# Kernel optimization log

Hardware: AMD Instinct MI355X
Metric: run time of the kernel (lower is better)

Reference implementation:

```python
import jax, jax.numpy as jnp
import numpy as np
from jax import lax

B, CIN, H, W = 4096, 3, 64, 64
NVAR = 50

def _lin(x, w, b):
    return jax.nn.relu(x @ w + b)

def setup_inputs() -> dict:
    key = jax.random.key(0)
    ks = jax.random.split(key, 16)
    def rn(k, shape, scale=0.05):
        return jax.random.normal(k, shape, dtype=jnp.float32) * scale
    return {
        "x": jax.random.normal(ks[0], (B, CIN, H, W), dtype=jnp.float32),
        "C": jax.random.uniform(ks[1], (B, NVAR, NVAR), dtype=jnp.float32),
        "conv1_w": rn(ks[2], (32, CIN, 3, 3)), "conv1_b": jnp.zeros((32,), jnp.float32),
        "conv2_w": rn(ks[3], (64, 32, 3, 3)), "conv2_b": jnp.zeros((64,), jnp.float32),
        "enc_w": rn(ks[4], (64, 128)), "enc_b": jnp.zeros((128,), jnp.float32),
        "f1_w": rn(ks[5], (128, NVAR)), "f1_b": jnp.zeros((NVAR,), jnp.float32),
        "f2_w": rn(ks[6], (NVAR, 128)), "f2_b": jnp.zeros((128,), jnp.float32),
        "f3_w": rn(ks[7], (256, 64)), "f3_b": jnp.zeros((64,), jnp.float32),
        "f4_w": rn(ks[8], (64, 64)), "f4_b": jnp.zeros((64,), jnp.float32),
        "f5_w": rn(ks[9], (64, 64)), "f5_b": jnp.zeros((64,), jnp.float32),
        "out_w": rn(ks[10], (64, NVAR)), "out_b": jnp.zeros((NVAR,), jnp.float32),
    }

def reference(x, C, conv1_w, conv1_b, conv2_w, conv2_b, enc_w, enc_b,
              f1_w, f1_b, f2_w, f2_b, f3_w, f3_b, f4_w, f4_b, f5_w, f5_b,
              out_w, out_b):
    dn = ("NCHW", "OIHW", "NCHW")
    # Observation_Encoder_F: conv(s2)->relu->conv(s2)->relu->global mean pool->linear->relu
    h = lax.conv_general_dilated(x, conv1_w, (2, 2), ((1, 1), (1, 1)), dimension_numbers=dn)
    h = jax.nn.relu(h + conv1_b[None, :, None, None])          # [B,32,32,32]
    h = lax.conv_general_dilated(h, conv2_w, (2, 2), ((1, 1), (1, 1)), dimension_numbers=dn)
    h = jax.nn.relu(h + conv2_b[None, :, None, None])          # [B,64,16,16]
    x1 = _lin(h.mean(axis=(2, 3)), enc_w, enc_b)               # [B,128]
    x2 = _lin(x1, f1_w, f1_b)                                  # [B,V]
    # per-sample causal matrix multiply: e[b] = C[b] @ x2[b]
    e = jnp.einsum("bij,bj->bi", C, x2)                        # [B,V]
    x3 = _lin(e, f2_w, f2_b)                                   # [B,128]
    x4 = jnp.concatenate((x1, x3), axis=1)                     # [B,256]
    x5 = _lin(x4, f3_w, f3_b)
    x6 = _lin(x5, f4_w, f4_b)
    x7 = _lin(x6, f5_w, f5_b)
    return jax.nn.softmax(_lin(x7, out_w, out_b), axis=1)      # [B,V]
```

## Files before the change

### kernel.cpp

```cpp
#include <hip/hip_runtime.h>
#include <hip/hip_bf16.h>


typedef __attribute__((ext_vector_type(8)))  short short8;
typedef __attribute__((ext_vector_type(16))) float floatx16;

#define AS1 __attribute__((address_space(1)))
#define AS3 __attribute__((address_space(3)))

#define BAR_LGKM() asm volatile("s_waitcnt lgkmcnt(0)\ns_barrier" ::: "memory")
#define BAR_FULL() asm volatile("s_waitcnt vmcnt(0) lgkmcnt(0)\ns_barrier" ::: "memory")

__device__ __forceinline__ short f2bf(float f) {
    unsigned u = __float_as_uint(f);
    u += 0x7fffu + ((u >> 16) & 1u);
    return (short)(u >> 16);
}

__device__ __forceinline__ float rl(float v, int i) {
    return __int_as_float(__builtin_amdgcn_readlane(__float_as_int(v), i));
}

__device__ __forceinline__ unsigned pkbf2(float a, float b) {
    float2 fp; fp.x = a; fp.y = b;
    __hip_bfloat162 bb = __float22bfloat162_rn(fp);
    return *(unsigned*)&bb;
}

__global__ void k_prep(const float* __restrict__ cw2, const float* __restrict__ cw1,
                       short* __restrict__ packw) {
    const int idx = blockIdx.x * 256 + threadIdx.x;
    if (idx < 9 * 64 * 32) {
        const int ic  = idx & 31;
        const int oc  = (idx >> 5) & 63;
        const int pos = idx >> 11;
        packw[idx] = f2bf(cw2[oc * 288 + ic * 9 + pos]);
    } else if (idx < 9 * 64 * 32 + 32 * 32) {
        const int j  = idx - 9 * 64 * 32;
        const int k  = j & 31;
        const int oc = j >> 5;
        packw[idx] = (k < 27) ? f2bf(cw1[oc * 27 + k]) : (short)0;
    }
}

#define XS_OFF  0
#define A1_OFF  49152
#define A1STR   80
#define H1_OFF  90112
#define ROWB    2064
#define SMEM_SZ (49152 + 40960 + 66048)
#define SPB     16

__global__ __launch_bounds__(256, 1) void k_conv(
    const float* __restrict__ x,    const float* __restrict__ c1b,
    const short* __restrict__ packw, const float* __restrict__ c2b,
    float* __restrict__ pooled)
{
    __shared__ __align__(16) char smem[SMEM_SZ];
    float* xs      = (float*)(smem + XS_OFF);
    char*  a1      = smem + A1_OFF;
    char*  h1b     = smem + H1_OFF;
    float* poolbuf = (float*)(smem + A1_OFF);

    const int tid  = threadIdx.x;
    const int lane = tid & 63;
    const int w    = tid >> 6;

    const int col = lane & 31;
    const int ss  = lane >> 5;

    const int nt  = w & 1;
    const int mh  = w >> 1;
    const int ox2 = lane & 15;
    const int oyb = (lane >> 4) & 1;
    const int ocn = nt * 32 + col;
    const float bias2 = c2b[ocn];
    const float bias1 = c1b[col];

    short8 z8;
    #pragma unroll
    for (int i = 0; i < 8; ++i) z8[i] = 0;

    short8 bfr[9][2];
    #pragma unroll
    for (int pos = 0; pos < 9; ++pos)
        #pragma unroll
        for (int h = 0; h < 2; ++h)
            bfr[pos][h] = *(const short8*)(packw + (pos * 64 + ocn) * 32 + h * 16 + ss * 8);

    const short* w1p = packw + 18432;
    short8 w1f[2];
    #pragma unroll
    for (int k = 0; k < 2; ++k)
        w1f[k] = *(const short8*)(w1p + col * 32 + k * 16 + ss * 8);

    auto prefetch_x = [&](int bb) {
        const char* g = (const char*)(x + (size_t)bb * 12288);
        #pragma unroll
        for (int i = 0; i < 12; ++i) {
            const int off = (w * 12 + i) << 10;
            __builtin_amdgcn_global_load_lds(
                (const AS1 unsigned int*)(g + off + lane * 16),
                (AS3 unsigned int*)(smem + XS_OFF + off), 16, 0, 0);
        }
    };

    auto im2col = [&](int half) {
        #pragma unroll
        for (int px = 0; px < 2; ++px) {
            const int p  = tid + px * 256;
            const int oy = half * 16 + (p >> 5);
            const int ox = p & 31;
            float f[32];
            #pragma unroll
            for (int ic = 0; ic < 3; ++ic) {
                #pragma unroll
                for (int ky = 0; ky < 3; ++ky) {
                    const int  iy   = 2 * oy + ky - 1;
                    const bool oky  = iy >= 0;
                    const int  base = ic * 4096 + (oky ? iy : 0) * 64 + 2 * ox;
                    const float2 p12 = *(const float2*)(xs + base);
                    const float  v0  = xs[(base > 0) ? base - 1 : 0];
                    const int k = ic * 9 + ky * 3;
                    f[k + 0] = (oky && ox > 0) ? v0 : 0.f;
                    f[k + 1] = oky ? p12.x : 0.f;
                    f[k + 2] = oky ? p12.y : 0.f;
                }
            }
            f[27] = 0.f; f[28] = 0.f; f[29] = 0.f; f[30] = 0.f; f[31] = 0.f;
            unsigned pk[16];
            #pragma unroll
            for (int t = 0; t < 16; ++t) pk[t] = pkbf2(f[2 * t], f[2 * t + 1]);
            uint4* dst = (uint4*)(a1 + p * A1STR);
            dst[0] = make_uint4(pk[0],  pk[1],  pk[2],  pk[3]);
            dst[1] = make_uint4(pk[4],  pk[5],  pk[6],  pk[7]);
            dst[2] = make_uint4(pk[8],  pk[9],  pk[10], pk[11]);
            dst[3] = make_uint4(pk[12], pk[13], pk[14], pk[15]);
        }
    };

    auto conv1_mfma = [&](int half) {
        #pragma unroll
        for (int i = 0; i < 4; ++i) {
            const int t = w * 4 + i;
            const char* abase = a1 + (t * 32 + col) * A1STR + ss * 16;
            const short8 af0 = *(const short8*)(abase);
            const short8 af1 = *(const short8*)(abase + 32);
            floatx16 acc;
            #pragma unroll
            for (int r = 0; r < 16; ++r) acc[r] = 0.f;
            acc = __builtin_amdgcn_mfma_f32_32x32x16_bf16(af0, w1f[0], acc, 0, 0, 0);
            acc = __builtin_amdgcn_mfma_f32_32x32x16_bf16(af1, w1f[1], acc, 0, 0, 0);
            const int oyg = half * 16 + t;
            char* hb = h1b + oyg * ROWB + col * 2;
            #pragma unroll
            for (int r = 0; r < 16; r += 2) {
                const int row = (r & 3) + 8 * (r >> 2) + 4 * ss;
                const unsigned u = pkbf2(fmaxf(acc[r]     + bias1, 0.f),
                                         fmaxf(acc[r + 1] + bias1, 0.f));
                *(unsigned short*)(hb + (row >> 1) * 64)        = (unsigned short)u;
                *(unsigned short*)(hb + (row >> 1) * 64 + 1024) = (unsigned short)(u >> 16);
            }
        }
    };

    prefetch_x(blockIdx.x);

    #pragma unroll 1
    for (int s = 0; s < SPB; ++s) {
        const int b = blockIdx.x + (s << 8);

        BAR_FULL();
        im2col(0);
        BAR_LGKM();
        conv1_mfma(0);
        BAR_LGKM();
        im2col(1);
        BAR_LGKM();
        if (s + 1 < SPB) prefetch_x(blockIdx.x + ((s + 1) << 8));
        conv1_mfma(1);
        BAR_LGKM();

        float pool = 0.f;
        #pragma unroll
        for (int tp = 0; tp < 2; ++tp) {
            const int t0 = mh * 4 + tp * 2;
            floatx16 acc0, acc1;
            #pragma unroll
            for (int r = 0; r < 16; ++r) { acc0[r] = 0.f; acc1[r] = 0.f; }
            #pragma unroll
            for (int ky = 0; ky < 3; ++ky) {
                #pragma unroll
                for (int kx = 0; kx < 3; ++kx) {
                    const int  iy0 = t0 * 4 + oyb * 2 + ky - 1;
                    const int  ph  = (kx + 1) & 1;
                    const int  xh  = ox2 - (kx == 0 ? 1 : 0);
                    const bool okx = (xh >= 0);
                    const bool ok0 = okx && (iy0 >= 0);
                    const int  sb  = (ph * 16 + xh) * 64 + ss * 16;
                    const int  ba0 = iy0 * ROWB + sb;
                    const int  ba1 = ba0 + 4 * ROWB;
                    #pragma unroll
                    for (int h = 0; h < 2; ++h) {
                        short8 a0v = ok0 ? *(const short8*)(h1b + ba0 + h * 32) : z8;
                        short8 a1v = okx ? *(const short8*)(h1b + ba1 + h * 32) : z8;
                        const short8 bf = bfr[ky * 3 + kx][h];
                        acc0 = __builtin_amdgcn_mfma_f32_32x32x16_bf16(a0v, bf, acc0, 0, 0, 0);
                        acc1 = __builtin_amdgcn_mfma_f32_32x32x16_bf16(a1v, bf, acc1, 0, 0, 0);
                    }
                }
            }
            #pragma unroll
            for (int r = 0; r < 16; ++r) {
                pool += fmaxf(acc0[r] + bias2, 0.f);
                pool += fmaxf(acc1[r] + bias2, 0.f);
            }
        }
        pool += __shfl_xor(pool, 32, 64);
        if (lane < 32) poolbuf[w * 32 + lane] = pool;
        BAR_LGKM();
        if (tid < 64) {
            const int g = tid >> 5, c = tid & 31;
            pooled[(size_t)b * 64 + tid] =
                (poolbuf[g * 32 + c] + poolbuf[(g + 2) * 32 + c]) * (1.f / 256.f);
        }
    }
}

__global__ __launch_bounds__(256, 4) void k_mlp(
    const float* __restrict__ pooled, const float* __restrict__ C,
    const float* __restrict__ ew, const float* __restrict__ eb,
    const float* __restrict__ w1, const float* __restrict__ b1,
    const float* __restrict__ w2, const float* __restrict__ b2,
    const float* __restrict__ w3, const float* __restrict__ b3,
    const float* __restrict__ w4, const float* __restrict__ b4,
    const float* __restrict__ w5, const float* __restrict__ b5,
    const float* __restrict__ ow, const float* __restrict__ ob,
    float* __restrict__ out)
{
    const int lane = threadIdx.x & 63;
    const int w    = threadIdx.x >> 6;
    const int b    = blockIdx.x * 4 + w;
    const int jc   = (lane < 50) ? lane : 0;

    const float p0 = pooled[(size_t)b * 64 + lane];

    float x1a = eb[lane], x1b = eb[lane + 64];
    #pragma unroll 8
    for (int i = 0; i < 64; ++i) {
        const float ai = rl(p0, i);
        x1a += ai * ew[i * 128 + lane];
        x1b += ai * ew[i * 128 + 64 + lane];
    }
    x1a = fmaxf(x1a, 0.f); x1b = fmaxf(x1b, 0.f);

    float x2 = b1[jc];
    #pragma unroll 8
    for (int i = 0; i < 64; ++i)  x2 += rl(x1a, i) * w1[i * 50 + jc];
    #pragma unroll 8
    for (int i = 0; i < 64; ++i)  x2 += rl(x1b, i) * w1[(64 + i) * 50 + jc];
    x2 = fmaxf(x2, 0.f);

    const float2* C2 = (const float2*)(C + (size_t)b * 2500 + jc * 50);
    float e = 0.f;
    #pragma unroll 5
    for (int j = 0; j < 25; ++j) {
        const float2 cc = C2[j];
        e += cc.x * rl(x2, 2 * j) + cc.y * rl(x2, 2 * j + 1);
    }

    float x3a = b2[lane], x3b = b2[lane + 64];
    #pragma unroll 10
    for (int i = 0; i < 50; ++i) {
        const float ai = rl(e, i);
        x3a += ai * w2[i * 128 + lane];
        x3b += ai * w2[i * 128 + 64 + lane];
    }
    x3a = fmaxf(x3a, 0.f); x3b = fmaxf(x3b, 0.f);

    float x5 = b3[lane];
    #pragma unroll 8
    for (int i = 0; i < 64; ++i) x5 += rl(x1a, i) * w3[(i      ) * 64 + lane];
    #pragma unroll 8
    for (int i = 0; i < 64; ++i) x5 += rl(x1b, i) * w3[(64  + i) * 64 + lane];
    #pragma unroll 8
    for (int i = 0; i < 64; ++i) x5 += rl(x3a, i) * w3[(128 + i) * 64 + lane];
    #pragma unroll 8
    for (int i = 0; i < 64; ++i) x5 += rl(x3b, i) * w3[(192 + i) * 64 + lane];
    x5 = fmaxf(x5, 0.f);

    float x6 = b4[lane];
    #pragma unroll 8
    for (int i = 0; i < 64; ++i) x6 += rl(x5, i) * w4[i * 64 + lane];
    x6 = fmaxf(x6, 0.f);
    float x7 = b5[lane];
    #pragma unroll 8
    for (int i = 0; i < 64; ++i) x7 += rl(x6, i) * w5[i * 64 + lane];
    x7 = fmaxf(x7, 0.f);

    float lg = ob[jc];
    #pragma unroll 8
    for (int i = 0; i < 64; ++i) lg += rl(x7, i) * ow[i * 50 + jc];
    float z = (lane < 50) ? fmaxf(lg, 0.f) : -1e30f;

    float m = z;
    #pragma unroll
    for (int o = 32; o > 0; o >>= 1) m = fmaxf(m, __shfl_xor(m, o, 64));
    float pr = __expf(z - m);
    float sden = pr;
    #pragma unroll
    for (int o = 32; o > 0; o >>= 1) sden += __shfl_xor(sden, o, 64);

    if (lane < 50) out[(size_t)b * 50 + lane] = pr / sden;
}

extern "C" void kernel_launch(void* const* d_in, const int* in_sizes, int n_in,
                              void* d_out, int out_size, void* d_ws, size_t ws_size,
                              hipStream_t stream) {
    (void)in_sizes; (void)n_in; (void)out_size; (void)ws_size;
    const float* x   = (const float*)d_in[0];
    const float* Cm  = (const float*)d_in[1];
    const float* c1w = (const float*)d_in[2];
    const float* c1b = (const float*)d_in[3];
    const float* c2w = (const float*)d_in[4];
    const float* c2b = (const float*)d_in[5];
    const float* ew  = (const float*)d_in[6];
    const float* ebv = (const float*)d_in[7];
    const float* f1w = (const float*)d_in[8];
    const float* f1b = (const float*)d_in[9];
    const float* f2w = (const float*)d_in[10];
    const float* f2b = (const float*)d_in[11];
    const float* f3w = (const float*)d_in[12];
    const float* f3b = (const float*)d_in[13];
    const float* f4w = (const float*)d_in[14];
    const float* f4b = (const float*)d_in[15];
    const float* f5w = (const float*)d_in[16];
    const float* f5b = (const float*)d_in[17];
    const float* ow  = (const float*)d_in[18];
    const float* ob  = (const float*)d_in[19];

    short* packw  = (short*)d_ws;
    float* pooled = (float*)((char*)d_ws + 65536);
    float* out    = (float*)d_out;

    hipLaunchKernelGGL(k_prep, dim3(76),   dim3(256), 0, stream, c2w, c1w, packw);
    hipLaunchKernelGGL(k_conv, dim3(256),  dim3(256), 0, stream, x, c1b, packw, c2b, pooled);
    hipLaunchKernelGGL(k_mlp,  dim3(1024), dim3(256), 0, stream, pooled, Cm,
                       ew, ebv, f1w, f1b, f2w, f2b, f3w, f3b, f4w, f4b, f5w, f5b,
                       ow, ob, out);
}
```

Baseline: 430.7 us.

## Double conv block to 512 threads, swizzle conv1 output layout, transpose conv1 MFMA

Widens the conv kernel from 4 to 8 waves per block so each wave handles half the im2col pixels, conv1 tiles and conv2 row tiles, with pooling reduced across 8 partial sums. The conv1 MFMA operands are swapped so each lane holds consecutive output channels, letting it write packed 32-bit bf16 pairs into an XOR-swizzled h1 layout instead of scattered 16-bit stores. Conv2 reads use matching precomputed swizzled offsets, aiming to cut LDS bank conflicts and store counts. The larger block raises register pressure per wave, and with 156KB of LDS only one block fits per CU despite the launch bound of 2.

Measured after the change: 396.6 us. 7.9% less time.

```diff
diff --git a/kernel.cpp b/kernel.cpp
--- a/kernel.cpp
+++ b/kernel.cpp
@@ -51,7 +51,7 @@
 #define SMEM_SZ (49152 + 40960 + 66048)
 #define SPB     16
 
-__global__ __launch_bounds__(256, 1) void k_conv(
+__global__ __launch_bounds__(512, 2) void k_conv(
     const float* __restrict__ x,    const float* __restrict__ c1b,
     const short* __restrict__ packw, const float* __restrict__ c2b,
     float* __restrict__ pooled)
@@ -70,12 +70,10 @@
     const int ss  = lane >> 5;
 
     const int nt  = w & 1;
-    const int mh  = w >> 1;
     const int ox2 = lane & 15;
     const int oyb = (lane >> 4) & 1;
     const int ocn = nt * 32 + col;
     const float bias2 = c2b[ocn];
-    const float bias1 = c1b[col];
 
     short8 z8;
     #pragma unroll
@@ -94,11 +92,34 @@
     for (int k = 0; k < 2; ++k)
         w1f[k] = *(const short8*)(w1p + col * 32 + k * 16 + ss * 8);
 
+    float2 b1p[8];
+    #pragma unroll
+    for (int rp = 0; rp < 8; ++rp)
+        b1p[rp] = *(const float2*)(c1b + ((rp & 1) * 2 + (rp >> 1) * 8 + 4 * ss));
+
+    int  sbv[3][2];
+    bool okx[3];
+    #pragma unroll
+    for (int kx = 0; kx < 3; ++kx) {
+        const int ph   = (kx + 1) & 1;
+        const int xh   = ox2 - (kx == 0 ? 1 : 0);
+        const int slot = ph * 16 + xh;
+        const int swz  = (slot >> 1) & 3;
+        okx[kx] = (xh >= 0);
+        #pragma unroll
+        for (int h = 0; h < 2; ++h)
+            sbv[kx][h] = slot * 64 + (((ss + 2 * h) ^ swz) << 4);
+    }
+
+    const int slotpx = ((col & 1) << 4) + (col >> 1);
+    const int wswz   = (slotpx >> 1) & 3;
+    const int wbase  = slotpx * 64 + ss * 8;
+
     auto prefetch_x = [&](int bb) {
         const char* g = (const char*)(x + (size_t)bb * 12288);
         #pragma unroll
-        for (int i = 0; i < 12; ++i) {
-            const int off = (w * 12 + i) << 10;
+        for (int i = 0; i < 6; ++i) {
+            const int off = (w * 6 + i) << 10;
             __builtin_amdgcn_global_load_lds(
                 (const AS1 unsigned int*)(g + off + lane * 16),
                 (AS3 unsigned int*)(smem + XS_OFF + off), 16, 0, 0);
@@ -106,60 +127,56 @@
     };
 
     auto im2col = [&](int half) {
-        #pragma unroll
-        for (int px = 0; px < 2; ++px) {
-            const int p  = tid + px * 256;
-            const int oy = half * 16 + (p >> 5);
-            const int ox = p & 31;
-            float f[32];
+        const int p  = tid;
+        const int oy = half * 16 + (p >> 5);
+        const int ox = p & 31;
+        float f[32];
+        #pragma unroll
+        for (int ic = 0; ic < 3; ++ic) {
             #pragma unroll
-            for (int ic = 0; ic < 3; ++ic) {
-                #pragma unroll
-                for (int ky = 0; ky < 3; ++ky) {
-                    const int  iy   = 2 * oy + ky - 1;
-                    const bool oky  = iy >= 0;
-                    const int  base = ic * 4096 + (oky ? iy : 0) * 64 + 2 * ox;
-                    const float2 p12 = *(const float2*)(xs + base);
-                    const float  v0  = xs[(base > 0) ? base - 1 : 0];
-                    const int k = ic * 9 + ky * 3;
-                    f[k + 0] = (oky && ox > 0) ? v0 : 0.f;
-                    f[k + 1] = oky ? p12.x : 0.f;
-                    f[k + 2] = oky ? p12.y : 0.f;
-                }
+            for (int ky = 0; ky < 3; ++ky) {
+                const int  iy   = 2 * oy + ky - 1;
+                const bool oky  = iy >= 0;
+                const int  base = ic * 4096 + (oky ? iy : 0) * 64 + 2 * ox;
+                const float2 p12 = *(const float2*)(xs + base);
+                const float2 pm  = *(const float2*)(xs + (base >= 2 ? base - 2 : 0));
+                const int k = ic * 9 + ky * 3;
+                f[k + 0] = (oky && ox > 0) ? pm.y : 0.f;
+                f[k + 1] = oky ? p12.x : 0.f;
+                f[k + 2] = oky ? p12.y : 0.f;
             }
-            f[27] = 0.f; f[28] = 0.f; f[29] = 0.f; f[30] = 0.f; f[31] = 0.f;
-            unsigned pk[16];
-            #pragma unroll
-            for (int t = 0; t < 16; ++t) pk[t] = pkbf2(f[2 * t], f[2 * t + 1]);
-            uint4* dst = (uint4*)(a1 + p * A1STR);
-            dst[0] = make_uint4(pk[0],  pk[1],  pk[2],  pk[3]);
-            dst[1] = make_uint4(pk[4],  pk[5],  pk[6],  pk[7]);
-            dst[2] = make_uint4(pk[8],  pk[9],  pk[10], pk[11]);
-            dst[3] = make_uint4(pk[12], pk[13], pk[14], pk[15]);
-        }
+        }
+        f[27] = 0.f; f[28] = 0.f; f[29] = 0.f; f[30] = 0.f; f[31] = 0.f;
+        unsigned pk[16];
+        #pragma unroll
+        for (int t = 0; t < 16; ++t) pk[t] = pkbf2(f[2 * t], f[2 * t + 1]);
+        uint4* dst = (uint4*)(a1 + p * A1STR);
+        dst[0] = make_uint4(pk[0],  pk[1],  pk[2],  pk[3]);
+        dst[1] = make_uint4(pk[4],  pk[5],  pk[6],  pk[7]);
+        dst[2] = make_uint4(pk[8],  pk[9],  pk[10], pk[11]);
+        dst[3] = make_uint4(pk[12], pk[13], pk[14], pk[15]);
     };
 
     auto conv1_mfma = [&](int half) {
         #pragma unroll
-        for (int i = 0; i < 4; ++i) {
-            const int t = w * 4 + i;
+        for (int i = 0; i < 2; ++i) {
+            const int t = w * 2 + i;
             const char* abase = a1 + (t * 32 + col) * A1STR + ss * 16;
-            const short8 af0 = *(const short8*)(abase);
-            const short8 af1 = *(const short8*)(abase + 32);
+            const short8 bf0 = *(const short8*)(abase);
+            const short8 bf1 = *(const short8*)(abase + 32);
             floatx16 acc;
             #pragma unroll
             for (int r = 0; r < 16; ++r) acc[r] = 0.f;
-            acc = __builtin_amdgcn_mfma_f32_32x32x16_bf16(af0, w1f[0], acc, 0, 0, 0);
-            acc = __builtin_amdgcn_mfma_f32_32x32x16_bf16(af1, w1f[1], acc, 0, 0, 0);
+            acc = __builtin_amdgcn_mfma_f32_32x32x16_bf16(w1f[0], bf0, acc, 0, 0, 0);
+            acc = __builtin_amdgcn_mfma_f32_32x32x16_bf16(w1f[1], bf1, acc, 0, 0, 0);
             const int oyg = half * 16 + t;
-            char* hb = h1b + oyg * ROWB + col * 2;
+            char* hb = h1b + oyg * ROWB + wbase;
             #pragma unroll
-            for (int r = 0; r < 16; r += 2) {
-                const int row = (r & 3) + 8 * (r >> 2) + 4 * ss;
-                const unsigned u = pkbf2(fmaxf(acc[r]     + bias1, 0.f),
-                                         fmaxf(acc[r + 1] + bias1, 0.f));
-                *(unsigned short*)(hb + (row >> 1) * 64)        = (unsigned short)u;
-                *(unsigned short*)(hb + (row >> 1) * 64 + 1024) = (unsigned short)(u >> 16);
+            for (int rp = 0; rp < 8; ++rp) {
+                const unsigned u = pkbf2(fmaxf(acc[2 * rp]     + b1p[rp].x, 0.f),
+                                         fmaxf(acc[2 * rp + 1] + b1p[rp].y, 0.f));
+                const int off = (((rp >> 1) ^ wswz) << 4) + (rp & 1) * 4;
+                *(unsigned*)(hb + off) = u;
             }
         }
     };
@@ -181,40 +198,35 @@
         conv1_mfma(1);
         BAR_LGKM();
 
+        const int t0 = w >> 1;
         float pool = 0.f;
-        #pragma unroll
-        for (int tp = 0; tp < 2; ++tp) {
-            const int t0 = mh * 4 + tp * 2;
-            floatx16 acc0, acc1;
+        floatx16 acc0, acc1;
+        #pragma unroll
+        for (int r = 0; r < 16; ++r) { acc0[r] = 0.f; acc1[r] = 0.f; }
+        #pragma unroll
+        for (int ky = 0; ky < 3; ++ky) {
             #pragma unroll
-            for (int r = 0; r < 16; ++r) { acc0[r] = 0.f; acc1[r] = 0.f; }
-            #pragma unroll
-            for (int ky = 0; ky < 3; ++ky) {
+            for (int kx = 0; kx < 3; ++kx) {
+                const int  iy0 = t0 * 4 + oyb * 2 + ky - 1;
+                const bool ok0 = okx[kx] && (iy0 >= 0);
+                const bool ok1 = okx[kx];
+                const int  ba0 = iy0 * ROWB;
+                const int  ba1 = ba0 + 16 * ROWB;
                 #pragma unroll
-                for (int kx = 0; kx < 3; ++kx) {
-                    const int  iy0 = t0 * 4 + oyb * 2 + ky - 1;
-                    const int  ph  = (kx + 1) & 1;
-                    const int  xh  = ox2 - (kx == 0 ? 1 : 0);
-                    const bool okx = (xh >= 0);
-                    const bool ok0 = okx && (iy0 >= 0);
-                    const int  sb  = (ph * 16 + xh) * 64 + ss * 16;
-                    const int  ba0 = iy0 * ROWB + sb;
-                    const int  ba1 = ba0 + 4 * ROWB;
-                    #pragma unroll
-                    for (int h = 0; h < 2; ++h) {
-                        short8 a0v = ok0 ? *(const short8*)(h1b + ba0 + h * 32) : z8;
-                        short8 a1v = okx ? *(const short8*)(h1b + ba1 + h * 32) : z8;
-                        const short8 bf = bfr[ky * 3 + kx][h];
-                        acc0 = __builtin_amdgcn_mfma_f32_32x32x16_bf16(a0v, bf, acc0, 0, 0, 0);
-                        acc1 = __builtin_amdgcn_mfma_f32_32x32x16_bf16(a1v, bf, acc1, 0, 0, 0);
-                    }
+                for (int h = 0; h < 2; ++h) {
+                    const int so = sbv[kx][h];
+                    short8 a0v = ok0 ? *(const short8*)(h1b + ba0 + so) : z8;
+                    short8 a1v = ok1 ? *(const short8*)(h1b + ba1 + so) : z8;
+                    const short8 bf = bfr[ky * 3 + kx][h];
+                    acc0 = __builtin_amdgcn_mfma_f32_32x32x16_bf16(a0v, bf, acc0, 0, 0, 0);
+                    acc1 = __builtin_amdgcn_mfma_f32_32x32x16_bf16(a1v, bf, acc1, 0, 0, 0);
                 }
             }
-            #pragma unroll
-            for (int r = 0; r < 16; ++r) {
-                pool += fmaxf(acc0[r] + bias2, 0.f);
-                pool += fmaxf(acc1[r] + bias2, 0.f);
-            }
+        }
+        #pragma unroll
+        for (int r = 0; r < 16; ++r) {
+            pool += fmaxf(acc0[r] + bias2, 0.f);
+            pool += fmaxf(acc1[r] + bias2, 0.f);
         }
         pool += __shfl_xor(pool, 32, 64);
         if (lane < 32) poolbuf[w * 32 + lane] = pool;
@@ -222,7 +234,8 @@
         if (tid < 64) {
             const int g = tid >> 5, c = tid & 31;
             pooled[(size_t)b * 64 + tid] =
-                (poolbuf[g * 32 + c] + poolbuf[(g + 2) * 32 + c]) * (1.f / 256.f);
+                (poolbuf[(g    ) * 32 + c] + poolbuf[(g + 2) * 32 + c] +
+                 poolbuf[(g + 4) * 32 + c] + poolbuf[(g + 6) * 32 + c]) * (1.f / 256.f);
         }
     }
 }
@@ -344,7 +357,7 @@
     float* out    = (float*)d_out;
 
     hipLaunchKernelGGL(k_prep, dim3(76),   dim3(256), 0, stream, c2w, c1w, packw);
-    hipLaunchKernelGGL(k_conv, dim3(256),  dim3(256), 0, stream, x, c1b, packw, c2b, pooled);
+    hipLaunchKernelGGL(k_conv, dim3(256),  dim3(512), 0, stream, x, c1b, packw, c2b, pooled);
     hipLaunchKernelGGL(k_mlp,  dim3(1024), dim3(256), 0, stream, pooled, Cm,
                        ew, ebv, f1w, f1b, f2w, f2b, f3w, f3b, f4w, f4b, f5w, f5b,
                        ow, ob, out);
```
